# Kernel tuning notes

Measured on AMD Instinct MI355X. Metric: run time of the kernel, lower is better.

Reference implementation:

```python
import jax, jax.numpy as jnp
import numpy as np

N = 50000      # nodes
E = 800000     # edges
NF = 16        # nfeature_dim
H = 128        # hidden_dim
OUT = 4        # output_dim


def _edge_conv(x, edge_index, W1, b1, W2, b2, aggr):
    """PyG EdgeConv: message = MLP(cat[x_i, x_j - x_i]) per edge, aggregate at target i.
    edge_index[0]=source j, edge_index[1]=target i."""
    src, dst = edge_index[0], edge_index[1]
    xi = x[dst]                                   # [E, F]
    xj = x[src]                                   # [E, F]
    h = jnp.concatenate([xi, xj - xi], axis=-1)   # [E, 2F]
    m = jax.nn.relu(h @ W1 + b1) @ W2 + b2        # [E, H]
    if aggr == 'max':
        out = jax.ops.segment_max(m, dst, num_segments=N)
        out = jnp.where(jnp.isfinite(out), out, 0.0)  # nodes with no in-edges -> 0
    else:  # mean
        s = jax.ops.segment_sum(m, dst, num_segments=N)
        cnt = jax.ops.segment_sum(jnp.ones((m.shape[0], 1), m.dtype), dst, num_segments=N)
        out = s / jnp.maximum(cnt, 1.0)
    return out


def setup_inputs() -> dict:
    key = jax.random.key(0)
    ks = jax.random.split(key, 20)
    s = 0.05
    inp = {
        'x': jax.random.normal(ks[0], (N, NF), dtype=jnp.float32),
        'edge_attr': jax.random.uniform(ks[1], (E, 1), dtype=jnp.float32) + 0.1,
        'edge_index': jax.random.randint(ks[2], (2, E), 0, N, dtype=jnp.int64),
        # conv0: Linear(2*NF->H), Linear(H->H)
        'W01': jax.random.normal(ks[3], (2 * NF, H), dtype=jnp.float32) * s,
        'b01': jnp.zeros((H,), jnp.float32),
        'W02': jax.random.normal(ks[4], (H, H), dtype=jnp.float32) * s,
        'b02': jnp.zeros((H,), jnp.float32),
        # conv1: Linear(2*H->H), Linear(H->H)
        'W11': jax.random.normal(ks[5], (2 * H, H), dtype=jnp.float32) * s,
        'b11': jnp.zeros((H,), jnp.float32),
        'W12': jax.random.normal(ks[6], (H, H), dtype=jnp.float32) * s,
        'b12': jnp.zeros((H,), jnp.float32),
        # conv2: Linear(2*H->H), Linear(H->H)
        'W21': jax.random.normal(ks[7], (2 * H, H), dtype=jnp.float32) * s,
        'b21': jnp.zeros((H,), jnp.float32),
        'W22': jax.random.normal(ks[8], (H, H), dtype=jnp.float32) * s,
        'b22': jnp.zeros((H,), jnp.float32),
        # final fc
        'Wf': jax.random.normal(ks[9], (H, OUT), dtype=jnp.float32) * s,
        'bf': jnp.zeros((OUT,), jnp.float32),
    }
    return inp


def reference(x, edge_attr, edge_index, W01, b01, W02, b02, W11, b11, W12, b12,
              W21, b21, W22, b22, Wf, bf):
    # edge_attr is only nan-checked in the original forward; unused in math.
    # dropout_rate = 0.0 -> identity (eval-mode reference).
    h = _edge_conv(x, edge_index, W01, b01, W02, b02, 'max')
    h = jax.nn.relu(h)
    h = _edge_conv(h, edge_index, W11, b11, W12, b12, 'mean')
    h = jax.nn.relu(h)
    h = _edge_conv(h, edge_index, W21, b21, W22, b22, 'mean')
    return h @ Wf + bf  # [N, OUT]
```

## Files before the change

### kernel.cpp

```cpp
#include <hip/hip_runtime.h>
#include <stdint.h>

#define NNODES 50000
#define NEDGES 800000
#define FDIM 16
#define HDIM 128
#define NPAD 50176
#define NCH 98
#define NBLK64 782

typedef __attribute__((ext_vector_type(8))) short short8;
typedef __attribute__((ext_vector_type(4))) float f32x4;

static constexpr size_t NH  = (size_t)NNODES * HDIM;
static constexpr size_t NHB = NH * sizeof(float);

static constexpr size_t OFF_BUF0  = 0;
static constexpr size_t OFF_BUF1  = NHB;
static constexpr size_t OFF_BUF2  = 2 * NHB;
static constexpr size_t OFF_BFB   = 3 * NHB;
static constexpr size_t OFF_CNT   = OFF_BFB + NH * 2;
static constexpr size_t OFF_CUR   = OFF_CNT + NPAD * 4;
static constexpr size_t OFF_CSUM  = OFF_CUR + NPAD * 4;
static constexpr size_t OFF_COFF  = OFF_CSUM + 512;
static constexpr size_t OFF_WFOLD = OFF_COFF + 512;
static constexpr size_t OFF_BFOLD = OFF_WFOLD + 2048;
static constexpr size_t OFF_FLAG  = OFF_BFOLD + 256;
static constexpr size_t OFF_SEDGE = OFF_FLAG + 256;
static constexpr size_t OFF_W02H  = OFF_SEDGE + (size_t)NEDGES * 8;
static constexpr size_t OFF_W02L  = OFF_W02H + 32768;
static constexpr size_t OFF_W12H  = OFF_W02L + 32768;
static constexpr size_t OFF_W12L  = OFF_W12H + 32768;
static constexpr size_t OFF_W11H  = OFF_W12L + 32768;
static constexpr size_t OFF_W11L  = OFF_W11H + 65536;
static constexpr size_t OFF_W21H  = OFF_W11L + 65536;
static constexpr size_t OFF_W21L  = OFF_W21H + 65536;

__device__ inline unsigned enc_f32(float m) {
  unsigned u = __float_as_uint(m);
  return (u & 0x80000000u) ? ~u : (u | 0x80000000u);
}

__device__ inline ushort bf16_rne(float v) {
  const unsigned u = __float_as_uint(v);
  return (ushort)((u + 0x7fffu + ((u >> 16) & 1u)) >> 16);
}

__device__ inline void bf16_split(float v, ushort& h, ushort& l) {
  unsigned u = __float_as_uint(v);
  unsigned hb = (u + 0x7fffu + ((u >> 16) & 1u)) & 0xffff0000u;
  h = (ushort)(hb >> 16);
  float r = v - __uint_as_float(hb);
  unsigned ur = __float_as_uint(r);
  l = (ushort)((ur + 0x7fffu + ((ur >> 16) & 1u)) >> 16);
}

__device__ inline void split8_tr(const float v[8], short8& hv, short8& lv) {
  unsigned hp[4], lp[4];
  #pragma unroll
  for (int k = 0; k < 4; ++k) {
    const unsigned u0 = __float_as_uint(v[2 * k]);
    const unsigned u1 = __float_as_uint(v[2 * k + 1]);
    const unsigned h0 = u0 & 0xffff0000u;
    const unsigned h1 = u1 & 0xffff0000u;
    const float r0 = v[2 * k]     - __uint_as_float(h0);
    const float r1 = v[2 * k + 1] - __uint_as_float(h1);
    hp[k] = h1 | (h0 >> 16);
    lp[k] = (__float_as_uint(r1) & 0xffff0000u) | (__float_as_uint(r0) >> 16);
  }
  hv = *(short8*)hp;
  lv = *(short8*)lp;
}

__device__ inline short8 cvtpk8_bf16(const float v[8]) {
  unsigned r[4];
  #pragma unroll
  for (int k = 0; k < 4; ++k)
    asm("v_cvt_pk_bf16_f32 %0, %1, %2" : "=v"(r[k]) : "v"(v[2 * k]), "v"(v[2 * k + 1]));
  return *(short8*)r;
}

__global__ __launch_bounds__(256) void k_init(const int* __restrict__ raw,
                                              int* __restrict__ flag,
                                              unsigned* __restrict__ cnt,
                                              unsigned* __restrict__ outenc) {
  const int i = blockIdx.x * 256 + threadIdx.x;
  outenc[i] = 0u;
  if (i < NPAD) cnt[i] = 0u;
  if (i == 0) {
    int is64 = 1;
    #pragma unroll
    for (int k = 1; k < 64; k += 2)
      if (raw[k] != 0) is64 = 0;
    *flag = is64;
  }
}

__global__ __launch_bounds__(256) void k_count(const int* __restrict__ raw,
                                               const int* __restrict__ flag,
                                               unsigned* __restrict__ cnt) {
  const size_t e = (size_t)blockIdx.x * 256 + threadIdx.x;
  const int d = (*flag) ? raw[2 * ((size_t)NEDGES + e)] : raw[NEDGES + e];
  atomicAdd(&cnt[d], 1u);
}

__global__ __launch_bounds__(256) void k_scan1(const unsigned* __restrict__ cnt,
                                               unsigned* __restrict__ csum) {
  __shared__ unsigned s[256];
  const int t = threadIdx.x, b = blockIdx.x;
  s[t] = cnt[b * 512 + t] + cnt[b * 512 + 256 + t];
  __syncthreads();
  for (int off = 128; off; off >>= 1) {
    if (t < off) s[t] += s[t + off];
    __syncthreads();
  }
  if (t == 0) csum[b] = s[0];
}

__global__ void k_scan2(const unsigned* __restrict__ csum,
                        unsigned* __restrict__ coff) {
  if (threadIdx.x == 0) {
    unsigned r = 0;
    for (int i = 0; i < NCH; ++i) { coff[i] = r; r += csum[i]; }
  }
}

__global__ __launch_bounds__(256) void k_scan3(const unsigned* __restrict__ cnt,
                                               const unsigned* __restrict__ coff,
                                               unsigned* __restrict__ cursor) {
  __shared__ unsigned s[256];
  const int t = threadIdx.x, b = blockIdx.x;
  const int base = b * 512;
  const unsigned c0 = cnt[base + 2 * t], c1 = cnt[base + 2 * t + 1];
  s[t] = c0 + c1;
  __syncthreads();
  for (int off = 1; off < 256; off <<= 1) {
    unsigned v = s[t];
    if (t >= off) v += s[t - off];
    __syncthreads();
    s[t] = v;
    __syncthreads();
  }
  const unsigned o = coff[b] + s[t] - (c0 + c1);
  cursor[base + 2 * t] = o;
  cursor[base + 2 * t + 1] = o + c0;
}

__global__ __launch_bounds__(256) void k_scatter(const int* __restrict__ raw,
                                                 const int* __restrict__ flag,
                                                 unsigned* __restrict__ cursor,
                                                 int2* __restrict__ sedge) {
  const size_t e = (size_t)blockIdx.x * 256 + threadIdx.x;
  int s, d;
  if (*flag) { s = raw[2 * e]; d = raw[2 * ((size_t)NEDGES + e)]; }
  else       { s = raw[e];     d = raw[NEDGES + e]; }
  const unsigned p = atomicAdd(&cursor[d], 1u);
  int2 sd; sd.x = s; sd.y = d;
  sedge[p] = sd;
}

__device__ inline void prepw_body(const float* __restrict__ W2,
                                  ushort* __restrict__ Whi,
                                  ushort* __restrict__ Wlo, int blk) {
  const int gid = blk * 256 + threadIdx.x;
  const int row = gid & 15;
  const int kg  = (gid >> 4) & 3;
  const int ks  = (gid >> 6) & 3;
  const int ct  = gid >> 8;
  const int col = ct * 16 + row;
  const int k0  = ks * 32 + kg * 8;
  short8 hv, lv;
  #pragma unroll
  for (int j = 0; j < 8; ++j) {
    ushort h, l;
    bf16_split(W2[(size_t)(k0 + j) * HDIM + col], h, l);
    hv[j] = (short)h; lv[j] = (short)l;
  }
  *(short8*)(Whi + (size_t)gid * 8) = hv;
  *(short8*)(Wlo + (size_t)gid * 8) = lv;
}

__device__ inline void packab_body(const float* __restrict__ W1,
                                   ushort* __restrict__ Whi,
                                   ushort* __restrict__ Wlo, int blk) {
  const int gid = blk * 256 + threadIdx.x;
  const int row = gid & 15;
  const int kg  = (gid >> 4) & 3;
  const int ks  = (gid >> 6) & 3;
  const int ct  = gid >> 8;
  const int col = ct * 16 + row;
  const int k0  = ks * 32 + kg * 8;
  short8 hv, lv;
  #pragma unroll
  for (int j = 0; j < 8; ++j) {
    const int k = k0 + j;
    float v;
    if (col < HDIM) v = W1[(size_t)k * HDIM + col] - W1[(size_t)(k + HDIM) * HDIM + col];
    else            v = W1[(size_t)(k + HDIM) * HDIM + (col - HDIM)];
    ushort h, l;
    bf16_split(v, h, l);
    hv[j] = (short)h; lv[j] = (short)l;
  }
  *(short8*)(Whi + (size_t)gid * 8) = hv;
  *(short8*)(Wlo + (size_t)gid * 8) = lv;
}

__global__ __launch_bounds__(256) void k_prep_all(
    const float* __restrict__ W02, const float* __restrict__ W12,
    const float* __restrict__ W11, const float* __restrict__ W21,
    const float* __restrict__ W22, const float* __restrict__ Wf,
    const float* __restrict__ b22, const float* __restrict__ bf,
    ushort* __restrict__ W02h, ushort* __restrict__ W02l,
    ushort* __restrict__ W12h, ushort* __restrict__ W12l,
    ushort* __restrict__ W11h, ushort* __restrict__ W11l,
    ushort* __restrict__ W21h, ushort* __restrict__ W21l,
    float* __restrict__ Wfold, float* __restrict__ bfold) {
  const int b = blockIdx.x;
  if (b < 8)       prepw_body(W02, W02h, W02l, b);
  else if (b < 16) prepw_body(W12, W12h, W12l, b - 8);
  else if (b < 32) packab_body(W11, W11h, W11l, b - 16);
  else if (b < 48) packab_body(W21, W21h, W21l, b - 32);
  else {
    const int t = (b - 48) * 256 + threadIdx.x;
    const int f = t >> 2, o = t & 3;
    float acc = 0.f;
    for (int h = 0; h < HDIM; ++h)
      acc = fmaf(W22[f * HDIM + h], Wf[h * 4 + o], acc);
    Wfold[t] = acc;
    if (t < 4) {
      float a = bf[t];
      for (int h = 0; h < HDIM; ++h) a = fmaf(b22[h], Wf[h * 4 + t], a);
      bfold[t] = a;
    }
  }
}

__global__ __launch_bounds__(256) void k_node_ab16(const float* __restrict__ x,
                                                   const float* __restrict__ W1,
                                                   const float* __restrict__ b1,
                                                   float* __restrict__ A,
                                                   ushort* __restrict__ Bb) {
  __shared__ float s_x[16 * FDIM];
  const int tid = threadIdx.x;
  const int nb = blockIdx.x * 16;
  s_x[tid] = x[(size_t)nb * FDIM + tid];
  __syncthreads();
  const int h = tid & 127;
  const int half = tid >> 7;
  float accA[8], accB[8];
  #pragma unroll
  for (int j = 0; j < 8; ++j) { accA[j] = 0.f; accB[j] = 0.f; }
  #pragma unroll 4
  for (int f = 0; f < FDIM; ++f) {
    const float wt = W1[f * HDIM + h];
    const float wb = W1[(f + FDIM) * HDIM + h];
    const float wd = wt - wb;
    #pragma unroll
    for (int j = 0; j < 8; ++j) {
      const float xv = s_x[(half * 8 + j) * FDIM + f];
      accA[j] = fmaf(xv, wd, accA[j]);
      accB[j] = fmaf(xv, wb, accB[j]);
    }
  }
  const float bias = b1[h];
  #pragma unroll
  for (int j = 0; j < 8; ++j) {
    const size_t idx = (size_t)(nb + half * 8 + j) * HDIM + h;
    A[idx] = accA[j] + bias;
    Bb[idx] = bf16_rne(accB[j]);
  }
}

__global__ __launch_bounds__(256) void k_node_ab_mfma(
    const unsigned* __restrict__ X, const ushort* __restrict__ Whi,
    const ushort* __restrict__ Wlo, const float* __restrict__ b1,
    float* __restrict__ A, ushort* __restrict__ Bb) {
  __shared__ __align__(16) ushort s_hi[64 * 128];
  __shared__ __align__(16) ushort s_lo[64 * 128];
  const int tid = threadIdx.x;
  const int nb = blockIdx.x * 64;

  #pragma unroll
  for (int it = 0; it < 4; ++it) {
    const int idx = tid + it * 256;
    const int row = idx >> 4;
    const int kg8 = idx & 15;
    const int n = nb + row;
    float v[8];
    if (n < NNODES) {
      const unsigned* p = X + (size_t)n * HDIM + kg8 * 8;
      const uint4 u0 = *(const uint4*)p;
      const uint4 u1 = *(const uint4*)(p + 4);
      const unsigned uu[8] = {u0.x, u0.y, u0.z, u0.w, u1.x, u1.y, u1.z, u1.w};
      #pragma unroll
      for (int j = 0; j < 8; ++j)
        v[j] = (uu[j] & 0x80000000u) ? __uint_as_float(uu[j] ^ 0x80000000u) : 0.f;
    } else {
      #pragma unroll
      for (int j = 0; j < 8; ++j) v[j] = 0.f;
    }
    short8 hv, lv;
    split8_tr(v, hv, lv);
    const int unit = row * 16 + (kg8 ^ (row & 15));
    *(short8*)(s_hi + unit * 8) = hv;
    *(short8*)(s_lo + unit * 8) = lv;
  }
  __syncthreads();

  const int l15 = tid & 15;
  const int l4  = (tid >> 4) & 3;
  const int w   = tid >> 6;

  f32x4 acc[4][4];
  #pragma unroll
  for (int rt = 0; rt < 4; ++rt)
    #pragma unroll
    for (int c = 0; c < 4; ++c)
      #pragma unroll
      for (int r = 0; r < 4; ++r) acc[rt][c][r] = 0.f;

  #pragma unroll
  for (int ks = 0; ks < 4; ++ks) {
    short8 wh[4], wl[4];
    #pragma unroll
    for (int ctl = 0; ctl < 4; ++ctl) {
      const int ct_g = w * 4 + ctl;
      const size_t u = ((size_t)(((ct_g * 4 + ks) * 4 + l4) * 16 + l15)) * 8;
      wh[ctl] = *(const short8*)(Whi + u);
      wl[ctl] = *(const short8*)(Wlo + u);
    }
    #pragma unroll
    for (int rt = 0; rt < 4; ++rt) {
      const int unit = (rt * 16 + l15) * 16 + ((ks * 4 + l4) ^ l15);
      const short8 ah = *(const short8*)(s_hi + unit * 8);
      const short8 al = *(const short8*)(s_lo + unit * 8);
      #pragma unroll
      for (int ctl = 0; ctl < 4; ++ctl) {
        acc[rt][ctl] = __builtin_amdgcn_mfma_f32_16x16x32_bf16(al, wh[ctl], acc[rt][ctl], 0, 0, 0);
        acc[rt][ctl] = __builtin_amdgcn_mfma_f32_16x16x32_bf16(ah, wl[ctl], acc[rt][ctl], 0, 0, 0);
        acc[rt][ctl] = __builtin_amdgcn_mfma_f32_16x16x32_bf16(ah, wh[ctl], acc[rt][ctl], 0, 0, 0);
      }
    }
  }

  #pragma unroll
  for (int ctl = 0; ctl < 4; ++ctl) {
    const int col_g = w * 64 + ctl * 16 + l15;
    if (col_g < HDIM) {
      const float bias = b1[col_g];
      #pragma unroll
      for (int rt = 0; rt < 4; ++rt)
        #pragma unroll
        for (int r = 0; r < 4; ++r) {
          const int n = nb + rt * 16 + l4 * 4 + r;
          if (n < NNODES) A[(size_t)n * HDIM + col_g] = acc[rt][ctl][r] + bias;
        }
    } else {
      const int cb = col_g - HDIM;
      #pragma unroll
      for (int rt = 0; rt < 4; ++rt)
        #pragma unroll
        for (int r = 0; r < 4; ++r) {
          const int n = nb + rt * 16 + l4 * 4 + r;
          if (n < NNODES) Bb[(size_t)n * HDIM + cb] = bf16_rne(acc[rt][ctl][r]);
        }
    }
  }
}

__global__ __launch_bounds__(256) void k_node_l2_fused(
    const float* __restrict__ S, const unsigned* __restrict__ cnt,
    const ushort* __restrict__ W12h, const ushort* __restrict__ W12l,
    const float* __restrict__ b12,
    const ushort* __restrict__ W21h, const ushort* __restrict__ W21l,
    const float* __restrict__ b21,
    float* __restrict__ A, ushort* __restrict__ Bb) {
  __shared__ __align__(16) ushort s_hi[64 * 128];
  __shared__ __align__(16) ushort s_lo[64 * 128];
  __shared__ float s_m[64 * 132];
  __shared__ float s_scale[64];
  __shared__ float s_alive[64];
  const int tid = threadIdx.x;
  const int nb = blockIdx.x * 64;
  if (tid < 64) {
    const int n = nb + tid;
    const unsigned c = (n < NNODES) ? cnt[n] : 0u;
    s_scale[tid] = c ? 1.f / (float)c : 0.f;
    s_alive[tid] = c ? 1.f : 0.f;
  }
  __syncthreads();

  #pragma unroll
  for (int it = 0; it < 4; ++it) {
    const int idx = tid + it * 256;
    const int row = idx >> 4;
    const int kg8 = idx & 15;
    const int n = nb + row;
    float v[8];
    if (n < NNODES) {
      const float sc = s_scale[row];
      const float* p = S + (size_t)n * HDIM + kg8 * 8;
      const float4 a0 = *(const float4*)p;
      const float4 a1 = *(const float4*)(p + 4);
      v[0] = a0.x * sc; v[1] = a0.y * sc; v[2] = a0.z * sc; v[3] = a0.w * sc;
      v[4] = a1.x * sc; v[5] = a1.y * sc; v[6] = a1.z * sc; v[7] = a1.w * sc;
    } else {
      #pragma unroll
      for (int j = 0; j < 8; ++j) v[j] = 0.f;
    }
    short8 hv, lv;
    split8_tr(v, hv, lv);
    const int unit = row * 16 + (kg8 ^ (row & 15));
    *(short8*)(s_hi + unit * 8) = hv;
    *(short8*)(s_lo + unit * 8) = lv;
  }
  __syncthreads();

  const int l15 = tid & 15;
  const int l4  = (tid >> 4) & 3;
  const int w   = tid >> 6;

  {
    f32x4 acc[4][2];
    #pragma unroll
    for (int rt = 0; rt < 4; ++rt)
      #pragma unroll
      for (int c = 0; c < 2; ++c)
        #pragma unroll
        for (int r = 0; r < 4; ++r) acc[rt][c][r] = 0.f;

    #pragma unroll
    for (int ks = 0; ks < 4; ++ks) {
      short8 wh[2], wl[2];
      #pragma unroll
      for (int ctl = 0; ctl < 2; ++ctl) {
        const int ct_g = w * 2 + ctl;
        const size_t u = ((size_t)(((ct_g * 4 + ks) * 4 + l4) * 16 + l15)) * 8;
        wh[ctl] = *(const short8*)(W12h + u);
        wl[ctl] = *(const short8*)(W12l + u);
      }
      #pragma unroll
      for (int rt = 0; rt < 4; ++rt) {
        const int unit = (rt * 16 + l15) * 16 + ((ks * 4 + l4) ^ l15);
        const short8 ah = *(const short8*)(s_hi + unit * 8);
        const short8 al = *(const short8*)(s_lo + unit * 8);
        #pragma unroll
        for (int ctl = 0; ctl < 2; ++ctl) {
          acc[rt][ctl] = __builtin_amdgcn_mfma_f32_16x16x32_bf16(al, wh[ctl], acc[rt][ctl], 0, 0, 0);
          acc[rt][ctl] = __builtin_amdgcn_mfma_f32_16x16x32_bf16(ah, wl[ctl], acc[rt][ctl], 0, 0, 0);
          acc[rt][ctl] = __builtin_amdgcn_mfma_f32_16x16x32_bf16(ah, wh[ctl], acc[rt][ctl], 0, 0, 0);
        }
      }
    }

    const float bb0 = b12[w * 32 + l15];
    const float bb1 = b12[w * 32 + 16 + l15];
    #pragma unroll
    for (int rt = 0; rt < 4; ++rt)
      #pragma unroll
      for (int ctl = 0; ctl < 2; ++ctl)
        #pragma unroll
        for (int r = 0; r < 4; ++r) {
          const int row = rt * 16 + l4 * 4 + r;
          s_m[row * 132 + w * 32 + ctl * 16 + l15] =
              fmaxf(acc[rt][ctl][r] + (ctl ? bb1 : bb0), 0.f) * s_alive[row];
        }
  }
  __syncthreads();

  #pragma unroll
  for (int it = 0; it < 4; ++it) {
    const int idx = tid + it * 256;
    const int row = idx >> 4;
    const int kg8 = idx & 15;
    const float* p = s_m + row * 132 + kg8 * 8;
    float v[8];
    const float4 a0 = *(const float4*)p;
    const float4 a1 = *(const float4*)(p + 4);
    v[0] = a0.x; v[1] = a0.y; v[2] = a0.z; v[3] = a0.w;
    v[4] = a1.x; v[5] = a1.y; v[6] = a1.z; v[7] = a1.w;
    short8 hv, lv;
    split8_tr(v, hv, lv);
    const int unit = row * 16 + (kg8 ^ (row & 15));
    *(short8*)(s_hi + unit * 8) = hv;
    *(short8*)(s_lo + unit * 8) = lv;
  }
  __syncthreads();

  f32x4 acc2[4][4];
  #pragma unroll
  for (int rt = 0; rt < 4; ++rt)
    #pragma unroll
    for (int c = 0; c < 4; ++c)
      #pragma unroll
      for (int r = 0; r < 4; ++r) acc2[rt][c][r] = 0.f;

  #pragma unroll
  for (int ks = 0; ks < 4; ++ks) {
    short8 wh[4], wl[4];
    #pragma unroll
    for (int ctl = 0; ctl < 4; ++ctl) {
      const int ct_g = w * 4 + ctl;
      const size_t u = ((size_t)(((ct_g * 4 + ks) * 4 + l4) * 16 + l15)) * 8;
      wh[ctl] = *(const short8*)(W21h + u);
      wl[ctl] = *(const short8*)(W21l + u);
    }
    #pragma unroll
    for (int rt = 0; rt < 4; ++rt) {
      const int unit = (rt * 16 + l15) * 16 + ((ks * 4 + l4) ^ l15);
      const short8 ah = *(const short8*)(s_hi + unit * 8);
      const short8 al = *(const short8*)(s_lo + unit * 8);
      #pragma unroll
      for (int ctl = 0; ctl < 4; ++ctl) {
        acc2[rt][ctl] = __builtin_amdgcn_mfma_f32_16x16x32_bf16(al, wh[ctl], acc2[rt][ctl], 0, 0, 0);
        acc2[rt][ctl] = __builtin_amdgcn_mfma_f32_16x16x32_bf16(ah, wl[ctl], acc2[rt][ctl], 0, 0, 0);
        acc2[rt][ctl] = __builtin_amdgcn_mfma_f32_16x16x32_bf16(ah, wh[ctl], acc2[rt][ctl], 0, 0, 0);
      }
    }
  }

  #pragma unroll
  for (int ctl = 0; ctl < 4; ++ctl) {
    const int col_g = w * 64 + ctl * 16 + l15;
    if (col_g < HDIM) {
      const float bias = b21[col_g];
      #pragma unroll
      for (int rt = 0; rt < 4; ++rt)
        #pragma unroll
        for (int r = 0; r < 4; ++r) {
          const int n = nb + rt * 16 + l4 * 4 + r;
          if (n < NNODES) A[(size_t)n * HDIM + col_g] = acc2[rt][ctl][r] + bias;
        }
    } else {
      const int cb = col_g - HDIM;
      #pragma unroll
      for (int rt = 0; rt < 4; ++rt)
        #pragma unroll
        for (int r = 0; r < 4; ++r) {
          const int n = nb + rt * 16 + l4 * 4 + r;
          if (n < NNODES) Bb[(size_t)n * HDIM + cb] = bf16_rne(acc2[rt][ctl][r]);
        }
    }
  }
}

__global__ __launch_bounds__(256) void k_edge_l0_mfma(
    const float* __restrict__ A0, const ushort* __restrict__ B0b,
    const int2* __restrict__ sedge,
    const ushort* __restrict__ Whi,
    const float* __restrict__ b2, unsigned* __restrict__ outenc) {
  __shared__ __align__(16) char s_un[4 * 64 * 17 * 4];
  __shared__ int s_dstA[64];
  __shared__ int s_srcA[64];
  ushort* s_t = (ushort*)s_un;
  float*  s_m = (float*)s_un;

  const int tid = threadIdx.x;
  const int eb = blockIdx.x * 64;
  if (tid < 64) {
    const int2 sd = sedge[eb + tid];
    s_srcA[tid] = sd.x;
    s_dstA[tid] = sd.y;
  }
  __syncthreads();

  #pragma unroll
  for (int it = 0; it < 4; ++it) {
    const int idx = tid + it * 256;
    const int e = idx >> 4;
    const int kg8 = idx & 15;
    const int k0 = kg8 * 8;
    const float* ap = A0 + (size_t)s_dstA[e] * HDIM + k0;
    const ushort* bp = B0b + (size_t)s_srcA[e] * HDIM + k0;
    const float4 a0 = *(const float4*)ap;
    const float4 a1 = *(const float4*)(ap + 4);
    const short8 b8 = *(const short8*)bp;
    const float af[8] = {a0.x, a0.y, a0.z, a0.w, a1.x, a1.y, a1.z, a1.w};
    float v[8];
    #pragma unroll
    for (int j = 0; j < 8; ++j) {
      const float bv = __uint_as_float(((unsigned)(ushort)b8[j]) << 16);
      v[j] = fmaxf(af[j] + bv, 0.f);
    }
    const short8 hv = cvtpk8_bf16(v);
    const int unit = e * 16 + (kg8 ^ (e & 15));
    *(short8*)(s_t + unit * 8) = hv;
  }
  __syncthreads();

  const int l15 = tid & 15;
  const int l4  = (tid >> 4) & 3;
  const int w   = tid >> 6;

  f32x4 acc[4][2];
  #pragma unroll
  for (int rt = 0; rt < 4; ++rt)
    #pragma unroll
    for (int c = 0; c < 2; ++c)
      #pragma unroll
      for (int r = 0; r < 4; ++r) acc[rt][c][r] = 0.f;

  #pragma unroll
  for (int ks = 0; ks < 4; ++ks) {
    short8 wh[2];
    #pragma unroll
    for (int ctl = 0; ctl < 2; ++ctl) {
      const int ct_g = w * 2 + ctl;
      const size_t u = ((size_t)(((ct_g * 4 + ks) * 4 + l4) * 16 + l15)) * 8;
      wh[ctl] = *(const short8*)(Whi + u);
    }
    #pragma unroll
    for (int rt = 0; rt < 4; ++rt) {
      const int e = rt * 16 + l15;
      const int unit = e * 16 + ((ks * 4 + l4) ^ l15);
      const short8 ah = *(const short8*)(s_t + unit * 8);
      #pragma unroll
      for (int ctl = 0; ctl < 2; ++ctl)
        acc[rt][ctl] = __builtin_amdgcn_mfma_f32_16x16x32_bf16(ah, wh[ctl], acc[rt][ctl], 0, 0, 0);
    }
  }
  __syncthreads();

  float* smw = s_m + w * (64 * 17);
  const int le = tid & 63;
  const int colw = le & 15;
  const int g = le >> 4;
  #pragma unroll
  for (int ctl = 0; ctl < 2; ++ctl) {
    const float bb = b2[w * 32 + ctl * 16 + l15];
    #pragma unroll
    for (int rt = 0; rt < 4; ++rt)
      #pragma unroll
      for (int r = 0; r < 4; ++r)
        smw[(rt * 16 + l4 * 4 + r) * 17 + l15] = acc[rt][ctl][r] + bb;
    const int e0 = g * 16;
    int curd = s_dstA[e0];
    float run = smw[e0 * 17 + colw];
    for (int e = e0 + 1; e < e0 + 16; ++e) {
      const int d = s_dstA[e];
      const float v = smw[e * 17 + colw];
      if (d == curd) run = fmaxf(run, v);
      else {
        atomicMax(outenc + (size_t)curd * HDIM + w * 32 + ctl * 16 + colw, enc_f32(run));
        curd = d; run = v;
      }
    }
    atomicMax(outenc + (size_t)curd * HDIM + w * 32 + ctl * 16 + colw, enc_f32(run));
  }
}

__global__ __launch_bounds__(256) void k_seg_mean(const float* __restrict__ A,
                                                  const ushort* __restrict__ B,
                                                  const int2* __restrict__ sedge,
                                                  const unsigned* __restrict__ endv,
                                                  const unsigned* __restrict__ cnt,
                                                  float* __restrict__ S) {
  const int tid = threadIdx.x;
  const int n = blockIdx.x * 4 + (tid >> 6);
  const int lane = tid & 63;
  const unsigned end = endv[n];
  unsigned e = end - cnt[n];
  const float2 a = *(const float2*)(A + (size_t)n * HDIM + lane * 2);
  float sx = 0.f, sy = 0.f;
  for (; e + 8 <= end; e += 8) {
    int s[8];
    #pragma unroll
    for (int k = 0; k < 8; ++k) s[k] = sedge[e + k].x;
    unsigned bv[8];
    #pragma unroll
    for (int k = 0; k < 8; ++k)
      bv[k] = *(const unsigned*)(B + (size_t)s[k] * HDIM + lane * 2);
    #pragma unroll
    for (int k = 0; k < 8; ++k) {
      sx += fmaxf(a.x + __uint_as_float(bv[k] << 16), 0.f);
      sy += fmaxf(a.y + __uint_as_float(bv[k] & 0xffff0000u), 0.f);
    }
  }
  for (; e + 2 <= end; e += 2) {
    const int s0 = sedge[e].x, s1 = sedge[e + 1].x;
    const unsigned b0 = *(const unsigned*)(B + (size_t)s0 * HDIM + lane * 2);
    const unsigned b1 = *(const unsigned*)(B + (size_t)s1 * HDIM + lane * 2);
    sx += fmaxf(a.x + __uint_as_float(b0 << 16), 0.f) +
          fmaxf(a.x + __uint_as_float(b1 << 16), 0.f);
    sy += fmaxf(a.y + __uint_as_float(b0 & 0xffff0000u), 0.f) +
          fmaxf(a.y + __uint_as_float(b1 & 0xffff0000u), 0.f);
  }
  for (; e < end; ++e) {
    const unsigned bv = *(const unsigned*)(B + (size_t)sedge[e].x * HDIM + lane * 2);
    sx += fmaxf(a.x + __uint_as_float(bv << 16), 0.f);
    sy += fmaxf(a.y + __uint_as_float(bv & 0xffff0000u), 0.f);
  }
  float2 o; o.x = sx; o.y = sy;
  *(float2*)(S + (size_t)n * HDIM + lane * 2) = o;
}

__global__ __launch_bounds__(256) void k_seg_final(const float* __restrict__ A,
                                                   const ushort* __restrict__ B,
                                                   const int2* __restrict__ sedge,
                                                   const unsigned* __restrict__ endv,
                                                   const unsigned* __restrict__ cnt,
                                                   const float* __restrict__ Wfold,
                                                   const float* __restrict__ bfold,
                                                   const float* __restrict__ bf,
                                                   float* __restrict__ out) {
  const int tid = threadIdx.x;
  const int n = blockIdx.x * 4 + (tid >> 6);
  const int lane = tid & 63;
  const unsigned deg = cnt[n];
  if (deg == 0) {
    if (lane == 0) {
      float4 o; o.x = bf[0]; o.y = bf[1]; o.z = bf[2]; o.w = bf[3];
      ((float4*)out)[n] = o;
    }
    return;
  }
  const unsigned end = endv[n];
  unsigned e = end - deg;
  const float2 a = *(const float2*)(A + (size_t)n * HDIM + lane * 2);
  float sx = 0.f, sy = 0.f;
  for (; e + 8 <= end; e += 8) {
    int s[8];
    #pragma unroll
    for (int k = 0; k < 8; ++k) s[k] = sedge[e + k].x;
    unsigned bv[8];
    #pragma unroll
    for (int k = 0; k < 8; ++k)
      bv[k] = *(const unsigned*)(B + (size_t)s[k] * HDIM + lane * 2);
    #pragma unroll
    for (int k = 0; k < 8; ++k) {
      sx += fmaxf(a.x + __uint_as_float(bv[k] << 16), 0.f);
      sy += fmaxf(a.y + __uint_as_float(bv[k] & 0xffff0000u), 0.f);
    }
  }
  for (; e < end; ++e) {
    const unsigned bv = *(const unsigned*)(B + (size_t)sedge[e].x * HDIM + lane * 2);
    sx += fmaxf(a.x + __uint_as_float(bv << 16), 0.f);
    sy += fmaxf(a.y + __uint_as_float(bv & 0xffff0000u), 0.f);
  }
  const float inv = 1.f / (float)deg;
  const float vx = sx * inv, vy = sy * inv;
  const float4 w0 = ((const float4*)Wfold)[lane * 2];
  const float4 w1 = ((const float4*)Wfold)[lane * 2 + 1];
  float p0 = fmaf(vx, w0.x, vy * w1.x);
  float p1 = fmaf(vx, w0.y, vy * w1.y);
  float p2 = fmaf(vx, w0.z, vy * w1.z);
  float p3 = fmaf(vx, w0.w, vy * w1.w);
  #pragma unroll
  for (int off = 32; off; off >>= 1) {
    p0 += __shfl_xor(p0, off);
    p1 += __shfl_xor(p1, off);
    p2 += __shfl_xor(p2, off);
    p3 += __shfl_xor(p3, off);
  }
  if (lane == 0) {
    float4 o;
    o.x = p0 + bfold[0]; o.y = p1 + bfold[1];
    o.z = p2 + bfold[2]; o.w = p3 + bfold[3];
    ((float4*)out)[n] = o;
  }
}

extern "C" void kernel_launch(void* const* d_in, const int* in_sizes, int n_in,
                              void* d_out, int out_size, void* d_ws, size_t ws_size,
                              hipStream_t stream) {
  const float* x   = (const float*)d_in[0];
  const int*   eidx = (const int*)d_in[2];
  const float* W01 = (const float*)d_in[3];
  const float* b01 = (const float*)d_in[4];
  const float* W02 = (const float*)d_in[5];
  const float* b02 = (const float*)d_in[6];
  const float* W11 = (const float*)d_in[7];
  const float* b11 = (const float*)d_in[8];
  const float* W12 = (const float*)d_in[9];
  const float* b12 = (const float*)d_in[10];
  const float* W21 = (const float*)d_in[11];
  const float* b21 = (const float*)d_in[12];
  const float* W22 = (const float*)d_in[13];
  const float* b22 = (const float*)d_in[14];
  const float* Wf  = (const float*)d_in[15];
  const float* bf  = (const float*)d_in[16];
  float* out = (float*)d_out;
  char* ws = (char*)d_ws;

  float* buf0 = (float*)(ws + OFF_BUF0);
  float* buf1 = (float*)(ws + OFF_BUF1);
  float* buf2 = (float*)(ws + OFF_BUF2);
  ushort* bufB = (ushort*)(ws + OFF_BFB);
  unsigned* cnt    = (unsigned*)(ws + OFF_CNT);
  unsigned* cursor = (unsigned*)(ws + OFF_CUR);
  unsigned* csum   = (unsigned*)(ws + OFF_CSUM);
  unsigned* coff   = (unsigned*)(ws + OFF_COFF);
  float* Wfold = (float*)(ws + OFF_WFOLD);
  float* bfold = (float*)(ws + OFF_BFOLD);
  int* flag  = (int*)(ws + OFF_FLAG);
  int2* sedge = (int2*)(ws + OFF_SEDGE);
  ushort* W02h = (ushort*)(ws + OFF_W02H);
  ushort* W02l = (ushort*)(ws + OFF_W02L);
  ushort* W12h = (ushort*)(ws + OFF_W12H);
  ushort* W12l = (ushort*)(ws + OFF_W12L);
  ushort* W11h = (ushort*)(ws + OFF_W11H);
  ushort* W11l = (ushort*)(ws + OFF_W11L);
  ushort* W21h = (ushort*)(ws + OFF_W21H);
  ushort* W21l = (ushort*)(ws + OFF_W21L);

  k_init<<<(int)(NH / 256), 256, 0, stream>>>(eidx, flag, cnt, (unsigned*)buf2);
  k_count<<<NEDGES / 256, 256, 0, stream>>>(eidx, flag, cnt);
  k_scan1<<<NCH, 256, 0, stream>>>(cnt, csum);
  k_scan2<<<1, 64, 0, stream>>>(csum, coff);
  k_scan3<<<NCH, 256, 0, stream>>>(cnt, coff, cursor);
  k_scatter<<<NEDGES / 256, 256, 0, stream>>>(eidx, flag, cursor, sedge);
  k_prep_all<<<50, 256, 0, stream>>>(W02, W12, W11, W21, W22, Wf, b22, bf,
                                     W02h, W02l, W12h, W12l, W11h, W11l,
                                     W21h, W21l, Wfold, bfold);

  k_node_ab16<<<NNODES / 16, 256, 0, stream>>>(x, W01, b01, buf0, bufB);
  k_edge_l0_mfma<<<NEDGES / 64, 256, 0, stream>>>(buf0, bufB, sedge,
                                                  W02h, b02, (unsigned*)buf2);

  k_node_ab_mfma<<<NBLK64, 256, 0, stream>>>((const unsigned*)buf2, W11h, W11l,
                                             b11, buf0, bufB);
  k_seg_mean<<<NNODES / 4, 256, 0, stream>>>(buf0, bufB, sedge, cursor, cnt, buf1);

  k_node_l2_fused<<<NBLK64, 256, 0, stream>>>(buf1, cnt, W12h, W12l, b12,
                                              W21h, W21l, b21, buf0, bufB);
  k_seg_final<<<NNODES / 4, 256, 0, stream>>>(buf0, bufB, sedge, cursor, cnt,
                                              Wfold, bfold, bf, out);

  (void)in_sizes; (void)n_in; (void)out_size; (void)ws_size;
}
```

Measured before the change: 444.6 us.

## Store layer-0 A in bf16, cooperatively load edge indices, unroll max-scan

Layer-0 node projection A is now stored in bf16 rather than fp32, which halves the per-edge gather bytes for the dst-side operand in the layer-0 edge kernel at the cost of extra rounding. The segmented-mean kernels now load up to 64 source indices with one coalesced wave load and broadcast them with shuffles, replacing the serial per-edge index reads. The layer-0 segmented max scan preloads destinations and values into registers and unrolls fully, which cuts LDS reads and branch divergence.

```diff
diff --git a/kernel.cpp b/kernel.cpp
--- a/kernel.cpp
+++ b/kernel.cpp
@@ -238,7 +238,7 @@
 __global__ __launch_bounds__(256) void k_node_ab16(const float* __restrict__ x,
                                                    const float* __restrict__ W1,
                                                    const float* __restrict__ b1,
-                                                   float* __restrict__ A,
+                                                   ushort* __restrict__ Ab,
                                                    ushort* __restrict__ Bb) {
   __shared__ float s_x[16 * FDIM];
   const int tid = threadIdx.x;
@@ -266,7 +266,7 @@
   #pragma unroll
   for (int j = 0; j < 8; ++j) {
     const size_t idx = (size_t)(nb + half * 8 + j) * HDIM + h;
-    A[idx] = accA[j] + bias;
+    Ab[idx] = bf16_rne(accA[j] + bias);
     Bb[idx] = bf16_rne(accB[j]);
   }
 }
@@ -545,7 +545,7 @@
 }
 
 __global__ __launch_bounds__(256) void k_edge_l0_mfma(
-    const float* __restrict__ A0, const ushort* __restrict__ B0b,
+    const ushort* __restrict__ A0b, const ushort* __restrict__ B0b,
     const int2* __restrict__ sedge,
     const ushort* __restrict__ Whi,
     const float* __restrict__ b2, unsigned* __restrict__ outenc) {
@@ -570,17 +570,14 @@
     const int e = idx >> 4;
     const int kg8 = idx & 15;
     const int k0 = kg8 * 8;
-    const float* ap = A0 + (size_t)s_dstA[e] * HDIM + k0;
-    const ushort* bp = B0b + (size_t)s_srcA[e] * HDIM + k0;
-    const float4 a0 = *(const float4*)ap;
-    const float4 a1 = *(const float4*)(ap + 4);
-    const short8 b8 = *(const short8*)bp;
-    const float af[8] = {a0.x, a0.y, a0.z, a0.w, a1.x, a1.y, a1.z, a1.w};
+    const short8 a8 = *(const short8*)(A0b + (size_t)s_dstA[e] * HDIM + k0);
+    const short8 b8 = *(const short8*)(B0b + (size_t)s_srcA[e] * HDIM + k0);
     float v[8];
     #pragma unroll
     for (int j = 0; j < 8; ++j) {
+      const float av = __uint_as_float(((unsigned)(ushort)a8[j]) << 16);
       const float bv = __uint_as_float(((unsigned)(ushort)b8[j]) << 16);
-      v[j] = fmaxf(af[j] + bv, 0.f);
+      v[j] = fmaxf(av + bv, 0.f);
     }
     const short8 hv = cvtpk8_bf16(v);
     const int unit = e * 16 + (kg8 ^ (e & 15));
@@ -625,6 +622,10 @@
   const int le = tid & 63;
   const int colw = le & 15;
   const int g = le >> 4;
+  const int e0 = g * 16;
+  int dd[16];
+  #pragma unroll
+  for (int e = 0; e < 16; ++e) dd[e] = s_dstA[e0 + e];
   #pragma unroll
   for (int ctl = 0; ctl < 2; ++ctl) {
     const float bb = b2[w * 32 + ctl * 16 + l15];
@@ -633,19 +634,20 @@
       #pragma unroll
       for (int r = 0; r < 4; ++r)
         smw[(rt * 16 + l4 * 4 + r) * 17 + l15] = acc[rt][ctl][r] + bb;
-    const int e0 = g * 16;
-    int curd = s_dstA[e0];
-    float run = smw[e0 * 17 + colw];
-    for (int e = e0 + 1; e < e0 + 16; ++e) {
-      const int d = s_dstA[e];
-      const float v = smw[e * 17 + colw];
-      if (d == curd) run = fmaxf(run, v);
-      else {
-        atomicMax(outenc + (size_t)curd * HDIM + w * 32 + ctl * 16 + colw, enc_f32(run));
-        curd = d; run = v;
-      }
-    }
-    atomicMax(outenc + (size_t)curd * HDIM + w * 32 + ctl * 16 + colw, enc_f32(run));
+    float vv[16];
+    #pragma unroll
+    for (int e = 0; e < 16; ++e) vv[e] = smw[(e0 + e) * 17 + colw];
+    unsigned* const ocol = outenc + w * 32 + ctl * 16 + colw;
+    int curd = dd[0];
+    float run = vv[0];
+    #pragma unroll
+    for (int e = 1; e < 16; ++e) {
+      const bool same = (dd[e] == curd);
+      if (!same) atomicMax(ocol + (size_t)curd * HDIM, enc_f32(run));
+      run = same ? fmaxf(run, vv[e]) : vv[e];
+      curd = dd[e];
+    }
+    atomicMax(ocol + (size_t)curd * HDIM, enc_f32(run));
   }
 }
 
@@ -659,36 +661,34 @@
   const int n = blockIdx.x * 4 + (tid >> 6);
   const int lane = tid & 63;
   const unsigned end = endv[n];
-  unsigned e = end - cnt[n];
+  const unsigned deg = cnt[n];
+  const unsigned start = end - deg;
   const float2 a = *(const float2*)(A + (size_t)n * HDIM + lane * 2);
   float sx = 0.f, sy = 0.f;
-  for (; e + 8 <= end; e += 8) {
-    int s[8];
-    #pragma unroll
-    for (int k = 0; k < 8; ++k) s[k] = sedge[e + k].x;
-    unsigned bv[8];
-    #pragma unroll
-    for (int k = 0; k < 8; ++k)
-      bv[k] = *(const unsigned*)(B + (size_t)s[k] * HDIM + lane * 2);
-    #pragma unroll
-    for (int k = 0; k < 8; ++k) {
-      sx += fmaxf(a.x + __uint_as_float(bv[k] << 16), 0.f);
-      sy += fmaxf(a.y + __uint_as_float(bv[k] & 0xffff0000u), 0.f);
-    }
-  }
-  for (; e + 2 <= end; e += 2) {
-    const int s0 = sedge[e].x, s1 = sedge[e + 1].x;
-    const unsigned b0 = *(const unsigned*)(B + (size_t)s0 * HDIM + lane * 2);
-    const unsigned b1 = *(const unsigned*)(B + (size_t)s1 * HDIM + lane * 2);
-    sx += fmaxf(a.x + __uint_as_float(b0 << 16), 0.f) +
-          fmaxf(a.x + __uint_as_float(b1 << 16), 0.f);
-    sy += fmaxf(a.y + __uint_as_float(b0 & 0xffff0000u), 0.f) +
-          fmaxf(a.y + __uint_as_float(b1 & 0xffff0000u), 0.f);
-  }
-  for (; e < end; ++e) {
-    const unsigned bv = *(const unsigned*)(B + (size_t)sedge[e].x * HDIM + lane * 2);
-    sx += fmaxf(a.x + __uint_as_float(bv << 16), 0.f);
-    sy += fmaxf(a.y + __uint_as_float(bv & 0xffff0000u), 0.f);
+  for (unsigned cb = start; cb < end; cb += 64) {
+    const int m = (int)((end - cb < 64u) ? (end - cb) : 64u);
+    int myidx = 0;
+    if (lane < m) myidx = sedge[cb + lane].x;
+    int k = 0;
+    for (; k + 8 <= m; k += 8) {
+      unsigned bv[8];
+      #pragma unroll
+      for (int j = 0; j < 8; ++j) {
+        const int id = __shfl(myidx, k + j);
+        bv[j] = *(const unsigned*)(B + (size_t)id * HDIM + lane * 2);
+      }
+      #pragma unroll
+      for (int j = 0; j < 8; ++j) {
+        sx += fmaxf(a.x + __uint_as_float(bv[j] << 16), 0.f);
+        sy += fmaxf(a.y + __uint_as_float(bv[j] & 0xffff0000u), 0.f);
+      }
+    }
+    for (; k < m; ++k) {
+      const int id = __shfl(myidx, k);
+      const unsigned bv = *(const unsigned*)(B + (size_t)id * HDIM + lane * 2);
+      sx += fmaxf(a.x + __uint_as_float(bv << 16), 0.f);
+      sy += fmaxf(a.y + __uint_as_float(bv & 0xffff0000u), 0.f);
+    }
   }
   float2 o; o.x = sx; o.y = sy;
   *(float2*)(S + (size_t)n * HDIM + lane * 2) = o;
@@ -715,27 +715,33 @@
     return;
   }
   const unsigned end = endv[n];
-  unsigned e = end - deg;
+  const unsigned start = end - deg;
   const float2 a = *(const float2*)(A + (size_t)n * HDIM + lane * 2);
   float sx = 0.f, sy = 0.f;
-  for (; e + 8 <= end; e += 8) {
-    int s[8];
-    #pragma unroll
-    for (int k = 0; k < 8; ++k) s[k] = sedge[e + k].x;
-    unsigned bv[8];
-    #pragma unroll
-    for (int k = 0; k < 8; ++k)
-      bv[k] = *(const unsigned*)(B + (size_t)s[k] * HDIM + lane * 2);
-    #pragma unroll
-    for (int k = 0; k < 8; ++k) {
-      sx += fmaxf(a.x + __uint_as_float(bv[k] << 16), 0.f);
-      sy += fmaxf(a.y + __uint_as_float(bv[k] & 0xffff0000u), 0.f);
-    }
-  }
-  for (; e < end; ++e) {
-    const unsigned bv = *(const unsigned*)(B + (size_t)sedge[e].x * HDIM + lane * 2);
-    sx += fmaxf(a.x + __uint_as_float(bv << 16), 0.f);
-    sy += fmaxf(a.y + __uint_as_float(bv & 0xffff0000u), 0.f);
+  for (unsigned cb = start; cb < end; cb += 64) {
+    const int m = (int)((end - cb < 64u) ? (end - cb) : 64u);
+    int myidx = 0;
+    if (lane < m) myidx = sedge[cb + lane].x;
+    int k = 0;
+    for (; k + 8 <= m; k += 8) {
+      unsigned bv[8];
+      #pragma unroll
+      for (int j = 0; j < 8; ++j) {
+        const int id = __shfl(myidx, k + j);
+        bv[j] = *(const unsigned*)(B + (size_t)id * HDIM + lane * 2);
+      }
+      #pragma unroll
+      for (int j = 0; j < 8; ++j) {
+        sx += fmaxf(a.x + __uint_as_float(bv[j] << 16), 0.f);
+        sy += fmaxf(a.y + __uint_as_float(bv[j] & 0xffff0000u), 0.f);
+      }
+    }
+    for (; k < m; ++k) {
+      const int id = __shfl(myidx, k);
+      const unsigned bv = *(const unsigned*)(B + (size_t)id * HDIM + lane * 2);
+      sx += fmaxf(a.x + __uint_as_float(bv << 16), 0.f);
+      sy += fmaxf(a.y + __uint_as_float(bv & 0xffff0000u), 0.f);
+    }
   }
   const float inv = 1.f / (float)deg;
   const float vx = sx * inv, vy = sy * inv;
@@ -813,8 +819,9 @@
                                      W02h, W02l, W12h, W12l, W11h, W11l,
                                      W21h, W21l, Wfold, bfold);
 
-  k_node_ab16<<<NNODES / 16, 256, 0, stream>>>(x, W01, b01, buf0, bufB);
-  k_edge_l0_mfma<<<NEDGES / 64, 256, 0, stream>>>(buf0, bufB, sedge,
+  ushort* A0b = (ushort*)buf0;
+  k_node_ab16<<<NNODES / 16, 256, 0, stream>>>(x, W01, b01, A0b, bufB);
+  k_edge_l0_mfma<<<NEDGES / 64, 256, 0, stream>>>(A0b, bufB, sedge,
                                                   W02h, b02, (unsigned*)buf2);
 
   k_node_ab_mfma<<<NBLK64, 256, 0, stream>>>((const unsigned*)buf2, W11h, W11l,
```

Result: faster. 433.7 us (-2.5%).
